# Optimization experiments

Measured on AMD Instinct MI355X. Metric: run time of the kernel, lower is better.

The kernel has to match this reference:

```python
import jax, jax.numpy as jnp
import numpy as np

DIM = 1024
HEADS = 16
DIM_HEAD = 64
INNER = HEADS * DIM_HEAD  # 1024


def setup_inputs() -> dict:
    key = jax.random.key(0)
    ks = jax.random.split(key, 5)
    B, N = 4, 2048
    x = jax.random.normal(ks[0], (B, N, DIM), dtype=jnp.float32)
    # nn.Linear weights stored as [out, in]; we keep [in, out] for x @ W
    s = 1.0 / np.sqrt(DIM)
    Wq = jax.random.uniform(ks[1], (DIM, INNER), jnp.float32, -s, s)
    Wkv = jax.random.uniform(ks[2], (DIM, 2 * INNER), jnp.float32, -s, s)
    so = 1.0 / np.sqrt(INNER)
    Wo = jax.random.uniform(ks[3], (INNER, DIM), jnp.float32, -so, so)
    bo = jax.random.uniform(ks[4], (DIM,), jnp.float32, -so, so)
    return {"x": x, "Wq": Wq, "Wkv": Wkv, "Wo": Wo, "bo": bo}


def reference(x, Wq, Wkv, Wo, bo):
    B, N, _ = x.shape
    scale = DIM_HEAD ** -0.5
    q = x @ Wq                      # [B, N, INNER]
    kv = x @ Wkv                    # [B, N, 2*INNER]
    k, v = jnp.split(kv, 2, axis=-1)

    def split_heads(t):
        return t.reshape(B, N, HEADS, DIM_HEAD).transpose(0, 2, 1, 3)  # b h n d

    q, k, v = map(split_heads, (q, k, v))
    dots = jnp.einsum('bhid,bhjd->bhij', q, k) * scale
    # causal mask: positions j > i filled with -inf
    causal = jnp.triu(jnp.ones((N, N), dtype=bool), k=1)
    dots = jnp.where(causal, -jnp.inf, dots)
    attn = jax.nn.softmax(dots, axis=-1)
    out = jnp.einsum('bhij,bhjd->bhid', attn, v)
    out = out.transpose(0, 2, 1, 3).reshape(B, N, INNER)
    return out @ Wo + bo
```

## Files before the change

kernel.cpp:

```cpp
#include <hip/hip_runtime.h>
#include <hip/hip_bf16.h>
#include <math.h>

typedef __attribute__((ext_vector_type(8))) short bf16x8;
typedef __attribute__((ext_vector_type(4))) float f32x4;

static __device__ inline ushort f2bf(float f) {
    union { float f; unsigned u; } v; v.f = f;
    unsigned r = (v.u + 0x7fff + ((v.u >> 16) & 1)) >> 16;
    return (ushort)r;
}

#define GLD_LDS(g, l) \
    __builtin_amdgcn_global_load_lds( \
        (const __attribute__((address_space(1))) void*)(g), \
        (__attribute__((address_space(3))) void*)(l), 16, 0, 0)

__global__ __launch_bounds__(256) void convert_x(
    const float* __restrict__ x, ushort* __restrict__ xb)
{
    const size_t i = ((size_t)blockIdx.x * 256 + threadIdx.x) * 8;
    float4 a = *(const float4*)(x + i);
    float4 b = *(const float4*)(x + i + 4);
    bf16x8 t;
    t[0] = (short)f2bf(a.x); t[1] = (short)f2bf(a.y);
    t[2] = (short)f2bf(a.z); t[3] = (short)f2bf(a.w);
    t[4] = (short)f2bf(b.x); t[5] = (short)f2bf(b.y);
    t[6] = (short)f2bf(b.z); t[7] = (short)f2bf(b.w);
    *(bf16x8*)(xb + i) = t;
}

__global__ __launch_bounds__(256) void prep_w(
    const float* __restrict__ Wq, const float* __restrict__ Wkv,
    const float* __restrict__ Wo, ushort* __restrict__ Wt)
{
    const int w = threadIdx.x >> 6;
    const int lane = threadIdx.x & 63;
    const int tile = blockIdx.x * 4 + w;
    const int r0 = (tile >> 4) << 6;
    const int k0 = (tile & 15) << 6;

    const float* src; int ld, c0;
    if (r0 < 1024)      { src = Wq;  ld = 1024; c0 = r0; }
    else if (r0 < 3072) { src = Wkv; ld = 2048; c0 = r0 - 1024; }
    else                { src = Wo;  ld = 1024; c0 = r0 - 3072; }

    ushort v[64];
    #pragma unroll
    for (int k = 0; k < 64; ++k)
        v[k] = f2bf(src[(size_t)(k0 + k) * ld + c0 + lane]);

    ushort* dst = Wt + (size_t)(r0 + lane) * 1024 + k0;
    #pragma unroll
    for (int k = 0; k < 64; k += 8) {
        bf16x8 t;
        #pragma unroll
        for (int j = 0; j < 8; ++j) t[j] = (short)v[k + j];
        *(bf16x8*)(dst + k) = t;
    }
}

#define GEMM_MAIN_LOOP(Aptr, Btptr)                                            \
    __shared__ ushort As[128 * 32];                                            \
    __shared__ ushort Bs[128 * 32];                                            \
    const int tid = threadIdx.x;                                               \
    const int lane = tid & 63;                                                 \
    const int w = tid >> 6;                                                    \
    const int l15 = lane & 15;                                                 \
    const int quad = lane >> 4;                                                \
    const int wm = w & 1, wn = w >> 1;                                         \
    const int rowBase = blockIdx.y * 128;                                      \
    const int colBase = blockIdx.x * 128;                                      \
    const int sRow = lane >> 2;                                                \
    const int sOff = (lane & 3) * 8;                                           \
    const ushort* aG0 = (Aptr) + (size_t)(rowBase + (w*2+0)*16 + sRow) * 1024 + sOff; \
    const ushort* aG1 = (Aptr) + (size_t)(rowBase + (w*2+1)*16 + sRow) * 1024 + sOff; \
    const ushort* bG0 = (Btptr) + (size_t)(colBase + (w*2+0)*16 + sRow) * 1024 + sOff; \
    const ushort* bG1 = (Btptr) + (size_t)(colBase + (w*2+1)*16 + sRow) * 1024 + sOff; \
    ushort* aL0 = As + (w*2+0)*512;                                            \
    ushort* aL1 = As + (w*2+1)*512;                                            \
    ushort* bL0 = Bs + (w*2+0)*512;                                            \
    ushort* bL1 = Bs + (w*2+1)*512;                                            \
    f32x4 acc[4][4];                                                           \
    _Pragma("unroll")                                                          \
    for (int i = 0; i < 4; ++i)                                                \
        _Pragma("unroll")                                                      \
        for (int j = 0; j < 4; ++j) acc[i][j] = (f32x4){0.f,0.f,0.f,0.f};      \
    for (int k0 = 0; k0 < 1024; k0 += 32) {                                    \
        __syncthreads();                                                       \
        GLD_LDS(aG0 + k0, aL0);                                                \
        GLD_LDS(aG1 + k0, aL1);                                                \
        GLD_LDS(bG0 + k0, bL0);                                                \
        GLD_LDS(bG1 + k0, bL1);                                                \
        __syncthreads();                                                       \
        bf16x8 af[4], bf[4];                                                   \
        _Pragma("unroll")                                                      \
        for (int mi = 0; mi < 4; ++mi)                                         \
            af[mi] = *(const bf16x8*)&As[(wm*64 + mi*16 + l15)*32 + quad*8];   \
        _Pragma("unroll")                                                      \
        for (int ni = 0; ni < 4; ++ni)                                         \
            bf[ni] = *(const bf16x8*)&Bs[(wn*64 + ni*16 + l15)*32 + quad*8];   \
        _Pragma("unroll")                                                      \
        for (int mi = 0; mi < 4; ++mi)                                         \
            _Pragma("unroll")                                                  \
            for (int ni = 0; ni < 4; ++ni)                                     \
                acc[mi][ni] = __builtin_amdgcn_mfma_f32_16x16x32_bf16(         \
                    af[mi], bf[ni], acc[mi][ni], 0, 0, 0);                     \
    }

__global__ __launch_bounds__(256) void gemm_qkv(
    const ushort* __restrict__ A, const ushort* __restrict__ Bt,
    ushort* __restrict__ Qb, ushort* __restrict__ Kb, ushort* __restrict__ Vt)
{
    GEMM_MAIN_LOOP(A, Bt)

    const int seg = colBase >> 10;
    if (seg == 2) {
        #pragma unroll
        for (int mi = 0; mi < 4; ++mi) {
            #pragma unroll
            for (int ni = 0; ni < 4; ++ni) {
                const int c = (colBase + wn*64 + ni*16 + l15) & 1023;
                const int h = c >> 6, d = c & 63;
                const int m = rowBase + wm*64 + mi*16 + quad*4;
                const int b = m >> 11, nn = m & 2047;
                ushort4 v;
                v.x = f2bf(acc[mi][ni][0]); v.y = f2bf(acc[mi][ni][1]);
                v.z = f2bf(acc[mi][ni][2]); v.w = f2bf(acc[mi][ni][3]);
                *(ushort4*)(Vt + ((size_t)(b*16 + h)*64 + d)*2048 + nn) = v;
            }
        }
    } else {
        ushort* dst = seg ? Kb : Qb;
        const float sc = seg ? 1.0f : 0.18033688011112042f;
        #pragma unroll
        for (int mi = 0; mi < 4; ++mi) {
            #pragma unroll
            for (int ni = 0; ni < 4; ++ni) {
                const int c = (colBase + wn*64 + ni*16 + l15) & 1023;
                const int h = c >> 6, d = c & 63;
                #pragma unroll
                for (int r = 0; r < 4; ++r) {
                    const int m = rowBase + wm*64 + mi*16 + quad*4 + r;
                    const int b = m >> 11, nn = m & 2047;
                    dst[((((size_t)b*16 + h)*2048 + nn) << 6) + d] = f2bf(acc[mi][ni][r] * sc);
                }
            }
        }
    }
}

__global__ __launch_bounds__(256) void gemm_out(
    const ushort* __restrict__ A, const ushort* __restrict__ Bt,
    const float* __restrict__ bo, float* __restrict__ out)
{
    GEMM_MAIN_LOOP(A, Bt)

    #pragma unroll
    for (int mi = 0; mi < 4; ++mi) {
        #pragma unroll
        for (int ni = 0; ni < 4; ++ni) {
            const int n = colBase + wn*64 + ni*16 + l15;
            const float bb = bo[n];
            #pragma unroll
            for (int r = 0; r < 4; ++r) {
                const int m = rowBase + wm*64 + mi*16 + quad*4 + r;
                out[(size_t)m * 1024 + n] = acc[mi][ni][r] + bb;
            }
        }
    }
}

__device__ __forceinline__ bf16x8 lds_frag(const ushort* S, int row, int chunk) {
    return *(const bf16x8*)(S + row * 64 + ((chunk ^ (row & 7)) << 3));
}

__global__ __launch_bounds__(256, 2) void flash_mfma(
    const ushort* __restrict__ Qb,
    const ushort* __restrict__ Kb,
    const ushort* __restrict__ Vt,
    ushort* __restrict__ Ob)
{
    __shared__ ushort Ks[2][4096];
    __shared__ ushort Vs[2][4096];
    __shared__ ushort PsAll[4][32][72];

    const int tid = threadIdx.x;
    const int w = tid >> 6;
    const int lane = tid & 63;
    const int l15 = lane & 15;
    const int quad = lane >> 4;
    ushort (*Ps)[72] = PsAll[w];

    const int blk = blockIdx.x;
    const int bh = ((blk & 7) << 3) | ((blk >> 3) & 7);
    const int qt = 15 - (blk >> 6);
    const int nt = 2 * qt + 2;
    const int rb0 = (qt << 7) + w * 32;

    const int sr0 = tid >> 3, sr1 = sr0 + 32;
    const int cg0 = (tid & 7) ^ (sr0 & 7);
    const int cg1 = (tid & 7) ^ (sr1 & 7);
    const ushort* kgb = Kb + (size_t)bh * 131072;
    const ushort* vgb = Vt + (size_t)bh * 131072;

    bf16x8 qf[2][2];
    #pragma unroll
    for (int mi = 0; mi < 2; ++mi) {
        const ushort* qp = Qb + ((size_t)bh * 2048 + rb0 + mi*16 + l15) * 64 + quad * 8;
        qf[mi][0] = *(const bf16x8*)qp;
        qf[mi][1] = *(const bf16x8*)(qp + 32);
    }

    bf16x8 bones;
    #pragma unroll
    for (int j = 0; j < 8; ++j) bones[j] = (short)0x3F80;

    float m_r[2];
    f32x4 o[2][4], lacc[2];
    #pragma unroll
    for (int mi = 0; mi < 2; ++mi) {
        m_r[mi] = -INFINITY;
        lacc[mi] = (f32x4){0.f, 0.f, 0.f, 0.f};
        #pragma unroll
        for (int nb = 0; nb < 4; ++nb) o[mi][nb] = (f32x4){0.f, 0.f, 0.f, 0.f};
    }

    GLD_LDS(kgb + sr0*64 + cg0*8, &Ks[0][tid*8]);
    GLD_LDS(kgb + sr1*64 + cg1*8, &Ks[0][tid*8 + 2048]);
    GLD_LDS(vgb + (size_t)sr0*2048 + cg0*8, &Vs[0][tid*8]);
    GLD_LDS(vgb + (size_t)sr1*2048 + cg1*8, &Vs[0][tid*8 + 2048]);

    for (int t = 0; t < nt; ++t) {
        __syncthreads();
        const int cur = t & 1;
        if (t + 1 < nt) {
            const int jn = t + 1;
            ushort* kd = &Ks[cur ^ 1][tid * 8];
            ushort* vd = &Vs[cur ^ 1][tid * 8];
            GLD_LDS(kgb + (size_t)jn*4096 + sr0*64 + cg0*8, kd);
            GLD_LDS(kgb + (size_t)jn*4096 + sr1*64 + cg1*8, kd + 2048);
            GLD_LDS(vgb + (size_t)sr0*2048 + jn*64 + cg0*8, vd);
            GLD_LDS(vgb + (size_t)sr1*2048 + jn*64 + cg1*8, vd + 2048);
        }
        const int j0 = t << 6;
        if (j0 > rb0 + 31) continue;

        const ushort* Ksb = Ks[cur];
        const ushort* Vsb = Vs[cur];

        f32x4 St[2][4];
        #pragma unroll
        for (int kb = 0; kb < 4; ++kb) {
            bf16x8 ka = lds_frag(Ksb, kb*16 + l15, quad);
            bf16x8 kc = lds_frag(Ksb, kb*16 + l15, quad + 4);
            #pragma unroll
            for (int mi = 0; mi < 2; ++mi) {
                f32x4 s = (f32x4){0.f, 0.f, 0.f, 0.f};
                s = __builtin_amdgcn_mfma_f32_16x16x32_bf16(ka, qf[mi][0], s, 0, 0, 0);
                s = __builtin_amdgcn_mfma_f32_16x16x32_bf16(kc, qf[mi][1], s, 0, 0, 0);
                St[mi][kb] = s;
            }
        }

        #pragma unroll
        for (int mi = 0; mi < 2; ++mi) {
            const int qrow = rb0 + mi*16 + l15;
            if (j0 + 63 > rb0 + mi*16) {
                #pragma unroll
                for (int kb = 0; kb < 4; ++kb) {
                    const int kbase = j0 + kb*16 + quad*4;
                    #pragma unroll
                    for (int r = 0; r < 4; ++r)
                        if (kbase + r > qrow) St[mi][kb][r] = -INFINITY;
                }
            }
            f32x4 mv = St[mi][0];
            #pragma unroll
            for (int kb = 1; kb < 4; ++kb)
                #pragma unroll
                for (int r = 0; r < 4; ++r) mv[r] = fmaxf(mv[r], St[mi][kb][r]);
            float mx = fmaxf(fmaxf(mv[0], mv[1]), fmaxf(mv[2], mv[3]));
            mx = fmaxf(mx, __shfl_xor(mx, 16));
            mx = fmaxf(mx, __shfl_xor(mx, 32));
            const float mold = m_r[mi];
            const float mnew = fmaxf(mold, mx);
            if (__any(mnew > mold)) {
                m_r[mi] = mnew;
                const float corr = __builtin_amdgcn_exp2f(mold - mnew);
                float ct[4];
                #pragma unroll
                for (int r = 0; r < 4; ++r) ct[r] = __shfl(corr, quad*4 + r);
                #pragma unroll
                for (int r = 0; r < 4; ++r) lacc[mi][r] *= ct[r];
                #pragma unroll
                for (int nb = 0; nb < 4; ++nb)
                    #pragma unroll
                    for (int r = 0; r < 4; ++r) o[mi][nb][r] *= ct[r];
            }
            #pragma unroll
            for (int kb = 0; kb < 4; ++kb)
                #pragma unroll
                for (int r = 0; r < 4; ++r)
                    St[mi][kb][r] = __builtin_amdgcn_exp2f(St[mi][kb][r] - mnew);
            #pragma unroll
            for (int kb = 0; kb < 4; ++kb) {
                union { float f; unsigned u; } c0, c1, c2, c3;
                c0.f = St[mi][kb][0]; c1.f = St[mi][kb][1];
                c2.f = St[mi][kb][2]; c3.f = St[mi][kb][3];
                uint2 pk;
                pk.x = (c0.u >> 16) | (c1.u & 0xFFFF0000u);
                pk.y = (c2.u >> 16) | (c3.u & 0xFFFF0000u);
                *(uint2*)&Ps[mi*16 + l15][kb*16 + quad*4] = pk;
            }
        }

        bf16x8 pf[2][2];
        #pragma unroll
        for (int mi = 0; mi < 2; ++mi) {
            pf[mi][0] = *(const bf16x8*)&Ps[mi*16 + l15][quad * 8];
            pf[mi][1] = *(const bf16x8*)&Ps[mi*16 + l15][32 + quad * 8];
        }
        #pragma unroll
        for (int mi = 0; mi < 2; ++mi) {
            lacc[mi] = __builtin_amdgcn_mfma_f32_16x16x32_bf16(pf[mi][0], bones, lacc[mi], 0, 0, 0);
            lacc[mi] = __builtin_amdgcn_mfma_f32_16x16x32_bf16(pf[mi][1], bones, lacc[mi], 0, 0, 0);
        }
        #pragma unroll
        for (int nb = 0; nb < 4; ++nb) {
            bf16x8 va = lds_frag(Vsb, nb*16 + l15, quad);
            bf16x8 vc = lds_frag(Vsb, nb*16 + l15, quad + 4);
            #pragma unroll
            for (int mi = 0; mi < 2; ++mi) {
                o[mi][nb] = __builtin_amdgcn_mfma_f32_16x16x32_bf16(pf[mi][0], va, o[mi][nb], 0, 0, 0);
                o[mi][nb] = __builtin_amdgcn_mfma_f32_16x16x32_bf16(pf[mi][1], vc, o[mi][nb], 0, 0, 0);
            }
        }
    }

    const int b = bh >> 4, h = bh & 15;
    #pragma unroll
    for (int mi = 0; mi < 2; ++mi)
        #pragma unroll
        for (int r = 0; r < 4; ++r) {
            const int ig = rb0 + mi*16 + quad*4 + r;
            const float inv = 1.f / lacc[mi][r];
            ushort* op = Ob + ((size_t)(b * 2048 + ig)) * 1024 + h * 64 + l15;
            #pragma unroll
            for (int nb = 0; nb < 4; ++nb)
                op[nb * 16] = f2bf(o[mi][nb][r] * inv);
        }
}

extern "C" void kernel_launch(void* const* d_in, const int* in_sizes, int n_in,
                              void* d_out, int out_size, void* d_ws, size_t ws_size,
                              hipStream_t stream) {
    const float* x   = (const float*)d_in[0];
    const float* Wq  = (const float*)d_in[1];
    const float* Wkv = (const float*)d_in[2];
    const float* Wo  = (const float*)d_in[3];
    const float* bo  = (const float*)d_in[4];
    float* out = (float*)d_out;

    const size_t SEG = (size_t)8388608 * 2;
    char* ws = (char*)d_ws;
    ushort* xb = (ushort*)(ws);
    ushort* Qb = (ushort*)(ws + SEG);
    ushort* Kb = (ushort*)(ws + SEG * 2);
    ushort* Vt = (ushort*)(ws + SEG * 3);
    ushort* Ob = (ushort*)(ws + SEG * 4);
    ushort* Wt = (ushort*)(ws + SEG * 5);

    convert_x<<<dim3(4096), 256, 0, stream>>>(x, xb);
    prep_w<<<dim3(256), 256, 0, stream>>>(Wq, Wkv, Wo, Wt);
    gemm_qkv<<<dim3(24, 64), 256, 0, stream>>>(xb, Wt, Qb, Kb, Vt);
    flash_mfma<<<dim3(1024), 256, 0, stream>>>(Qb, Kb, Vt, Ob);
    gemm_out<<<dim3(8, 64), 256, 0, stream>>>(Ob, Wt + (size_t)3072 * 1024, bo, out);
}
```

Before: 261.0 us.

## Rewrite GEMM main loop as double-buffered 128x256 pipelined MFMA with swizzled LDS

Replaces the simple 128x128, K=32 GEMM loop with a 512-thread, 128x256-tile, K=64 double-buffered pipeline. Global-to-LDS loads for the next stages are interleaved with MFMA phases, using explicit vmcnt waits, barriers and setprio. It adds an XOR-swizzled LDS layout to avoid bank conflicts and a workgroup remapping for L2 locality. The intent is to hide load latency and raise MFMA utilization in the QKV and output projections, at the cost of much more LDS per block, hand-tuned synchronization and possible register pressure under launch_bounds(512,2).

```diff
diff --git a/kernel.cpp b/kernel.cpp
--- a/kernel.cpp
+++ b/kernel.cpp
@@ -60,59 +60,103 @@
     }
 }
 
-#define GEMM_MAIN_LOOP(Aptr, Btptr)                                            \
-    __shared__ ushort As[128 * 32];                                            \
-    __shared__ ushort Bs[128 * 32];                                            \
+#define STG_A(t) { ushort* d_ = &As[(t) & 1][ldst];                            \
+    GLD_LDS(aS0 + (size_t)(t) * 64, d_);                                       \
+    GLD_LDS(aS1 + (size_t)(t) * 64, d_ + 64 * 64); }
+#define STG_B1(t) { ushort* d_ = &Bs[(t) & 1][ldst];                           \
+    GLD_LDS(bS0 + (size_t)(t) * 64, d_);                                       \
+    GLD_LDS(bS1 + (size_t)(t) * 64, d_ + 64 * 64); }
+#define STG_B2(t) { ushort* d_ = &Bs[(t) & 1][128 * 64 + ldst];                \
+    GLD_LDS(bS2 + (size_t)(t) * 64, d_);                                       \
+    GLD_LDS(bS3 + (size_t)(t) * 64, d_ + 64 * 64); }
+
+#define GEMM_PIPE(Aptr, Btptr, NXT, NWG)                                       \
+    __shared__ ushort As[2][128 * 64];                                         \
+    __shared__ ushort Bs[2][256 * 64];                                         \
     const int tid = threadIdx.x;                                               \
     const int lane = tid & 63;                                                 \
     const int w = tid >> 6;                                                    \
     const int l15 = lane & 15;                                                 \
     const int quad = lane >> 4;                                                \
-    const int wm = w & 1, wn = w >> 1;                                         \
-    const int rowBase = blockIdx.y * 128;                                      \
-    const int colBase = blockIdx.x * 128;                                      \
-    const int sRow = lane >> 2;                                                \
-    const int sOff = (lane & 3) * 8;                                           \
-    const ushort* aG0 = (Aptr) + (size_t)(rowBase + (w*2+0)*16 + sRow) * 1024 + sOff; \
-    const ushort* aG1 = (Aptr) + (size_t)(rowBase + (w*2+1)*16 + sRow) * 1024 + sOff; \
-    const ushort* bG0 = (Btptr) + (size_t)(colBase + (w*2+0)*16 + sRow) * 1024 + sOff; \
-    const ushort* bG1 = (Btptr) + (size_t)(colBase + (w*2+1)*16 + sRow) * 1024 + sOff; \
-    ushort* aL0 = As + (w*2+0)*512;                                            \
-    ushort* aL1 = As + (w*2+1)*512;                                            \
-    ushort* bL0 = Bs + (w*2+0)*512;                                            \
-    ushort* bL1 = Bs + (w*2+1)*512;                                            \
+    const int wm = w >> 2, wn = w & 3;                                         \
+    const int cx = l15 & 7;                                                    \
+    const int lin = blockIdx.y * (NXT) + blockIdx.x;                           \
+    const int wg = (lin & 7) * ((NWG) >> 3) + (lin >> 3);                      \
+    const int rowBase = (wg / (NXT)) * 128;                                    \
+    const int colBase = (wg % (NXT)) * 256;                                    \
+    const int sr = tid >> 3, sc = tid & 7;                                     \
+    const int ldst = sr * 64 + sc * 8;                                         \
+    const ushort* aS0 = (Aptr) + (size_t)(rowBase + sr) * 1024 + ((sc ^ (sr & 7)) << 3); \
+    const ushort* aS1 = aS0 + (size_t)64 * 1024;                               \
+    const ushort* bS0 = (Btptr) + (size_t)(colBase + sr) * 1024 + ((sc ^ (sr & 7)) << 3); \
+    const ushort* bS1 = bS0 + (size_t)64 * 1024;                               \
+    const ushort* bS2 = bS0 + (size_t)128 * 1024;                              \
+    const ushort* bS3 = bS0 + (size_t)192 * 1024;                              \
     f32x4 acc[4][4];                                                           \
     _Pragma("unroll")                                                          \
-    for (int i = 0; i < 4; ++i)                                                \
+    for (int i_ = 0; i_ < 4; ++i_)                                             \
         _Pragma("unroll")                                                      \
-        for (int j = 0; j < 4; ++j) acc[i][j] = (f32x4){0.f,0.f,0.f,0.f};      \
-    for (int k0 = 0; k0 < 1024; k0 += 32) {                                    \
-        __syncthreads();                                                       \
-        GLD_LDS(aG0 + k0, aL0);                                                \
-        GLD_LDS(aG1 + k0, aL1);                                                \
-        GLD_LDS(bG0 + k0, bL0);                                                \
-        GLD_LDS(bG1 + k0, bL1);                                                \
-        __syncthreads();                                                       \
-        bf16x8 af[4], bf[4];                                                   \
+        for (int j_ = 0; j_ < 4; ++j_) acc[i_][j_] = (f32x4){0.f, 0.f, 0.f, 0.f}; \
+    STG_A(0) STG_B1(0) STG_B2(0) STG_B1(1) STG_B2(1)                           \
+    asm volatile("s_waitcnt vmcnt(4)" ::: "memory");                           \
+    __builtin_amdgcn_s_barrier();                                              \
+    asm volatile("" ::: "memory");                                             \
+    _Pragma("unroll 1")                                                        \
+    for (int u = 0; u < 16; ++u) {                                             \
+        const ushort* aRd = &As[u & 1][(wm * 64 + l15) * 64];                  \
+        const ushort* bRd = &Bs[u & 1][(wn * 64 + l15) * 64];                  \
+        const int c0 = (quad ^ cx) << 3, c1 = ((4 | quad) ^ cx) << 3;          \
+        bf16x8 bF0[4], bF1[4];                                                 \
         _Pragma("unroll")                                                      \
-        for (int mi = 0; mi < 4; ++mi)                                         \
-            af[mi] = *(const bf16x8*)&As[(wm*64 + mi*16 + l15)*32 + quad*8];   \
+        for (int ni = 0; ni < 4; ++ni) {                                       \
+            bF0[ni] = *(const bf16x8*)(bRd + ni * 1024 + c0);                  \
+            bF1[ni] = *(const bf16x8*)(bRd + ni * 1024 + c1);                  \
+        }                                                                      \
+        bf16x8 a0 = *(const bf16x8*)(aRd + c0);                                \
+        bf16x8 a1 = *(const bf16x8*)(aRd + c1);                                \
+        if (u + 1 < 16) { STG_A(u + 1) }                                       \
+        __builtin_amdgcn_s_barrier();                                          \
+        asm volatile("s_waitcnt lgkmcnt(0)" ::: "memory");                     \
+        __builtin_amdgcn_sched_barrier(0);                                     \
+        __builtin_amdgcn_s_setprio(1);                                         \
         _Pragma("unroll")                                                      \
-        for (int ni = 0; ni < 4; ++ni)                                         \
-            bf[ni] = *(const bf16x8*)&Bs[(wn*64 + ni*16 + l15)*32 + quad*8];   \
+        for (int ni = 0; ni < 4; ++ni) {                                       \
+            acc[0][ni] = __builtin_amdgcn_mfma_f32_16x16x32_bf16(a0, bF0[ni], acc[0][ni], 0, 0, 0); \
+            acc[0][ni] = __builtin_amdgcn_mfma_f32_16x16x32_bf16(a1, bF1[ni], acc[0][ni], 0, 0, 0); \
+        }                                                                      \
+        __builtin_amdgcn_s_setprio(0);                                         \
+        __builtin_amdgcn_s_barrier();                                          \
+        asm volatile("" ::: "memory");                                         \
         _Pragma("unroll")                                                      \
-        for (int mi = 0; mi < 4; ++mi)                                         \
+        for (int q = 1; q < 4; ++q) {                                          \
+            bf16x8 aa = *(const bf16x8*)(aRd + q * 1024 + c0);                 \
+            bf16x8 ab = *(const bf16x8*)(aRd + q * 1024 + c1);                 \
+            if (q == 1 && u + 2 < 16) { STG_B1(u + 2) }                        \
+            if (q == 2 && u + 2 < 16) { STG_B2(u + 2) }                        \
+            __builtin_amdgcn_s_barrier();                                      \
+            asm volatile("s_waitcnt lgkmcnt(0)" ::: "memory");                 \
+            __builtin_amdgcn_sched_barrier(0);                                 \
+            __builtin_amdgcn_s_setprio(1);                                     \
             _Pragma("unroll")                                                  \
-            for (int ni = 0; ni < 4; ++ni)                                     \
-                acc[mi][ni] = __builtin_amdgcn_mfma_f32_16x16x32_bf16(         \
-                    af[mi], bf[ni], acc[mi][ni], 0, 0, 0);                     \
-    }
-
-__global__ __launch_bounds__(256) void gemm_qkv(
+            for (int ni = 0; ni < 4; ++ni) {                                   \
+                acc[q][ni] = __builtin_amdgcn_mfma_f32_16x16x32_bf16(aa, bF0[ni], acc[q][ni], 0, 0, 0); \
+                acc[q][ni] = __builtin_amdgcn_mfma_f32_16x16x32_bf16(ab, bF1[ni], acc[q][ni], 0, 0, 0); \
+            }                                                                  \
+            __builtin_amdgcn_s_setprio(0);                                     \
+            if (q == 3) {                                                      \
+                if (u < 14) { asm volatile("s_waitcnt vmcnt(4)" ::: "memory"); } \
+                else        { asm volatile("s_waitcnt vmcnt(0)" ::: "memory"); } \
+            }                                                                  \
+            __builtin_amdgcn_s_barrier();                                      \
+            asm volatile("" ::: "memory");                                     \
+        }                                                                      \
+    }
+
+__global__ __launch_bounds__(512, 2) void gemm_qkv(
     const ushort* __restrict__ A, const ushort* __restrict__ Bt,
     ushort* __restrict__ Qb, ushort* __restrict__ Kb, ushort* __restrict__ Vt)
 {
-    GEMM_MAIN_LOOP(A, Bt)
+    GEMM_PIPE(A, Bt, 12, 768)
 
     const int seg = colBase >> 10;
     if (seg == 2) {
@@ -132,7 +176,7 @@
         }
     } else {
         ushort* dst = seg ? Kb : Qb;
-        const float sc = seg ? 1.0f : 0.18033688011112042f;
+        const float sc2 = seg ? 1.0f : 0.18033688011112042f;
         #pragma unroll
         for (int mi = 0; mi < 4; ++mi) {
             #pragma unroll
@@ -143,18 +187,18 @@
                 for (int r = 0; r < 4; ++r) {
                     const int m = rowBase + wm*64 + mi*16 + quad*4 + r;
                     const int b = m >> 11, nn = m & 2047;
-                    dst[((((size_t)b*16 + h)*2048 + nn) << 6) + d] = f2bf(acc[mi][ni][r] * sc);
+                    dst[((((size_t)b*16 + h)*2048 + nn) << 6) + d] = f2bf(acc[mi][ni][r] * sc2);
                 }
             }
         }
     }
 }
 
-__global__ __launch_bounds__(256) void gemm_out(
+__global__ __launch_bounds__(512, 2) void gemm_out(
     const ushort* __restrict__ A, const ushort* __restrict__ Bt,
     const float* __restrict__ bo, float* __restrict__ out)
 {
-    GEMM_MAIN_LOOP(A, Bt)
+    GEMM_PIPE(A, Bt, 4, 256)
 
     #pragma unroll
     for (int mi = 0; mi < 4; ++mi) {
@@ -373,7 +417,7 @@
 
     convert_x<<<dim3(4096), 256, 0, stream>>>(x, xb);
     prep_w<<<dim3(256), 256, 0, stream>>>(Wq, Wkv, Wo, Wt);
-    gemm_qkv<<<dim3(24, 64), 256, 0, stream>>>(xb, Wt, Qb, Kb, Vt);
+    gemm_qkv<<<dim3(12, 64), 512, 0, stream>>>(xb, Wt, Qb, Kb, Vt);
     flash_mfma<<<dim3(1024), 256, 0, stream>>>(Qb, Kb, Vt, Ob);
-    gemm_out<<<dim3(8, 64), 256, 0, stream>>>(Ob, Wt + (size_t)3072 * 1024, bo, out);
-}
+    gemm_out<<<dim3(4, 64), 512, 0, stream>>>(Ob, Wt + (size_t)3072 * 1024, bo, out);
+}
```

New measurement: 248.6 us. 1.05x faster.

## Triple-buffer GEMM LDS loads with 128x256 tiles, 512 threads and XOR swizzle

Applied to the files above, without the earlier changes.

Replaces the single-buffered GEMM main loop with a three-stage LDS ring that prefetches two k-slices ahead and waits on vmcnt. A single barrier per iteration replaces the previous pair. Tiles grow to 128x256 with 8 waves per block, and linear block ids are remapped into a grouped order to improve L2 reuse. An XOR swizzle on the LDS chunk offsets reduces bank conflicts, and s_setprio is raised around the MFMA block. The trade-off is more LDS use (72KB per block) and fewer blocks in the grid (256 for the output GEMM), which can lower occupancy and leave CUs underused.

```diff
diff --git a/kernel.cpp b/kernel.cpp
--- a/kernel.cpp
+++ b/kernel.cpp
@@ -60,59 +60,80 @@
     }
 }
 
-#define GEMM_MAIN_LOOP(Aptr, Btptr)                                            \
-    __shared__ ushort As[128 * 32];                                            \
-    __shared__ ushort Bs[128 * 32];                                            \
+#define STG32(t, Ad, Bd) { \
+    GLD_LDS(aS + (size_t)(t) * 32, (Ad) + ldst); \
+    GLD_LDS(bSlo + (size_t)(t) * 32, (Bd) + ldst); \
+    GLD_LDS(bShi + (size_t)(t) * 32, (Bd) + 128 * 32 + ldst); }
+
+#define GEMM_PIPE(Aptr, Btptr, NXT, NWG)                                       \
+    __shared__ ushort As[3][128 * 32];                                         \
+    __shared__ ushort Bs[3][256 * 32];                                         \
     const int tid = threadIdx.x;                                               \
     const int lane = tid & 63;                                                 \
     const int w = tid >> 6;                                                    \
     const int l15 = lane & 15;                                                 \
     const int quad = lane >> 4;                                                \
-    const int wm = w & 1, wn = w >> 1;                                         \
-    const int rowBase = blockIdx.y * 128;                                      \
-    const int colBase = blockIdx.x * 128;                                      \
-    const int sRow = lane >> 2;                                                \
-    const int sOff = (lane & 3) * 8;                                           \
-    const ushort* aG0 = (Aptr) + (size_t)(rowBase + (w*2+0)*16 + sRow) * 1024 + sOff; \
-    const ushort* aG1 = (Aptr) + (size_t)(rowBase + (w*2+1)*16 + sRow) * 1024 + sOff; \
-    const ushort* bG0 = (Btptr) + (size_t)(colBase + (w*2+0)*16 + sRow) * 1024 + sOff; \
-    const ushort* bG1 = (Btptr) + (size_t)(colBase + (w*2+1)*16 + sRow) * 1024 + sOff; \
-    ushort* aL0 = As + (w*2+0)*512;                                            \
-    ushort* aL1 = As + (w*2+1)*512;                                            \
-    ushort* bL0 = Bs + (w*2+0)*512;                                            \
-    ushort* bL1 = Bs + (w*2+1)*512;                                            \
+    const int wm = w >> 2, wn = w & 3;                                         \
+    const int lin = blockIdx.y * (NXT) + blockIdx.x;                           \
+    const int wg = (lin & 7) * ((NWG) >> 3) + (lin >> 3);                      \
+    const int rowBase = (wg / (NXT)) * 128;                                    \
+    const int colBase = (wg % (NXT)) * 256;                                    \
+                         \
+    const int sr = tid >> 2, sc = tid & 3;                                     \
+    const int ldst = sr * 32 + sc * 8;                                         \
+    const int gsw = (sc ^ ((sr >> 1) & 3)) << 3;                               \
+    const ushort* aS   = (Aptr)  + (size_t)(rowBase + sr) * 1024 + gsw;        \
+    const ushort* bSlo = (Btptr) + (size_t)(colBase + sr) * 1024 + gsw;        \
+    const ushort* bShi = bSlo + (size_t)128 * 1024;                            \
+    \
+    const int co = ((quad ^ ((l15 >> 1) & 3)) << 3);                           \
     f32x4 acc[4][4];                                                           \
     _Pragma("unroll")                                                          \
-    for (int i = 0; i < 4; ++i)                                                \
+    for (int i_ = 0; i_ < 4; ++i_)                                             \
         _Pragma("unroll")                                                      \
-        for (int j = 0; j < 4; ++j) acc[i][j] = (f32x4){0.f,0.f,0.f,0.f};      \
-    for (int k0 = 0; k0 < 1024; k0 += 32) {                                    \
-        __syncthreads();                                                       \
-        GLD_LDS(aG0 + k0, aL0);                                                \
-        GLD_LDS(aG1 + k0, aL1);                                                \
-        GLD_LDS(bG0 + k0, bL0);                                                \
-        GLD_LDS(bG1 + k0, bL1);                                                \
-        __syncthreads();                                                       \
-        bf16x8 af[4], bf[4];                                                   \
+        for (int j_ = 0; j_ < 4; ++j_) acc[i_][j_] = (f32x4){0.f, 0.f, 0.f, 0.f}; \
+    ushort *Acur = As[0], *Anxt = As[1], *Apre = As[2];                        \
+    ushort *Bcur = Bs[0], *Bnxt = Bs[1], *Bpre = Bs[2];                        \
+    STG32(0, Acur, Bcur)                                                       \
+    STG32(1, Anxt, Bnxt)                                                       \
+    asm volatile("s_waitcnt vmcnt(3)" ::: "memory");                           \
+    __builtin_amdgcn_s_barrier();                                              \
+    asm volatile("" ::: "memory");                                             \
+    _Pragma("unroll 1")                                                        \
+    for (int u = 0; u < 32; ++u) {                                             \
+        if (u + 2 < 32) { STG32(u + 2, Apre, Bpre) }                           \
+        const ushort* aC = Acur + (wm * 64 + l15) * 32;                        \
+        const ushort* bC = Bcur + (wn * 64 + l15) * 32;                        \
+        bf16x8 aF[4], bF[4];                                                   \
+        _Pragma("unroll")                                                      \
+        for (int ni = 0; ni < 4; ++ni)                                         \
+            bF[ni] = *(const bf16x8*)(bC + ni * 512 + co);                     \
         _Pragma("unroll")                                                      \
         for (int mi = 0; mi < 4; ++mi)                                         \
-            af[mi] = *(const bf16x8*)&As[(wm*64 + mi*16 + l15)*32 + quad*8];   \
-        _Pragma("unroll")                                                      \
-        for (int ni = 0; ni < 4; ++ni)                                         \
-            bf[ni] = *(const bf16x8*)&Bs[(wn*64 + ni*16 + l15)*32 + quad*8];   \
+            aF[mi] = *(const bf16x8*)(aC + mi * 512 + co);                     \
+        __builtin_amdgcn_s_setprio(1);                                         \
         _Pragma("unroll")                                                      \
         for (int mi = 0; mi < 4; ++mi)                                         \
             _Pragma("unroll")                                                  \
             for (int ni = 0; ni < 4; ++ni)                                     \
                 acc[mi][ni] = __builtin_amdgcn_mfma_f32_16x16x32_bf16(         \
-                    af[mi], bf[ni], acc[mi][ni], 0, 0, 0);                     \
-    }
-
-__global__ __launch_bounds__(256) void gemm_qkv(
+                    aF[mi], bF[ni], acc[mi][ni], 0, 0, 0);                     \
+        __builtin_amdgcn_s_setprio(0);                                         \
+        if (u < 30)       { asm volatile("s_waitcnt vmcnt(3)" ::: "memory"); } \
+        else if (u == 30) { asm volatile("s_waitcnt vmcnt(0)" ::: "memory"); } \
+        if (u < 31) {                                                          \
+            __builtin_amdgcn_s_barrier();                                      \
+            asm volatile("" ::: "memory");                                     \
+        }                                                                      \
+        ushort* tA = Acur; Acur = Anxt; Anxt = Apre; Apre = tA;                \
+        ushort* tB = Bcur; Bcur = Bnxt; Bnxt = Bpre; Bpre = tB;                \
+    }
+
+__global__ __launch_bounds__(512, 4) void gemm_qkv(
     const ushort* __restrict__ A, const ushort* __restrict__ Bt,
     ushort* __restrict__ Qb, ushort* __restrict__ Kb, ushort* __restrict__ Vt)
 {
-    GEMM_MAIN_LOOP(A, Bt)
+    GEMM_PIPE(A, Bt, 12, 768)
 
     const int seg = colBase >> 10;
     if (seg == 2) {
@@ -132,7 +153,7 @@
         }
     } else {
         ushort* dst = seg ? Kb : Qb;
-        const float sc = seg ? 1.0f : 0.18033688011112042f;
+        const float sc2 = seg ? 1.0f : 0.18033688011112042f;
         #pragma unroll
         for (int mi = 0; mi < 4; ++mi) {
             #pragma unroll
@@ -143,18 +164,18 @@
                 for (int r = 0; r < 4; ++r) {
                     const int m = rowBase + wm*64 + mi*16 + quad*4 + r;
                     const int b = m >> 11, nn = m & 2047;
-                    dst[((((size_t)b*16 + h)*2048 + nn) << 6) + d] = f2bf(acc[mi][ni][r] * sc);
+                    dst[((((size_t)b*16 + h)*2048 + nn) << 6) + d] = f2bf(acc[mi][ni][r] * sc2);
                 }
             }
         }
     }
 }
 
-__global__ __launch_bounds__(256) void gemm_out(
+__global__ __launch_bounds__(512, 4) void gemm_out(
     const ushort* __restrict__ A, const ushort* __restrict__ Bt,
     const float* __restrict__ bo, float* __restrict__ out)
 {
-    GEMM_MAIN_LOOP(A, Bt)
+    GEMM_PIPE(A, Bt, 4, 256)
 
     #pragma unroll
     for (int mi = 0; mi < 4; ++mi) {
@@ -373,7 +394,7 @@
 
     convert_x<<<dim3(4096), 256, 0, stream>>>(x, xb);
     prep_w<<<dim3(256), 256, 0, stream>>>(Wq, Wkv, Wo, Wt);
-    gemm_qkv<<<dim3(24, 64), 256, 0, stream>>>(xb, Wt, Qb, Kb, Vt);
+    gemm_qkv<<<dim3(12, 64), 512, 0, stream>>>(xb, Wt, Qb, Kb, Vt);
     flash_mfma<<<dim3(1024), 256, 0, stream>>>(Qb, Kb, Vt, Ob);
-    gemm_out<<<dim3(8, 64), 256, 0, stream>>>(Ob, Wt + (size_t)3072 * 1024, bo, out);
-}
+    gemm_out<<<dim3(4, 64), 512, 0, stream>>>(Ob, Wt + (size_t)3072 * 1024, bo, out);
+}
```

Result: no change. 259.1 us (-0.7%).
